# Optimization experiments

Measured on AMD Instinct MI355X. Metric: run time of the kernel, lower is better.

## Reference

```python
import jax, jax.numpy as jnp
import numpy as np

B, S, D = 8, 1024, 768
H, DH = 8, 96          # number_of_heads, head_outdim = D // H
DFF = 4 * D            # mlp hidden
EPS = 1e-5


def _p(key, shape, scale=0.02):
    return (jax.random.normal(key, shape, dtype=jnp.float32) * scale)


def setup_inputs() -> dict:
    key = jax.random.key(0)
    ks = jax.random.split(key, 16)
    return {
        "h": jax.random.normal(ks[0], (B, S, D), dtype=jnp.float32),
        "x": jax.random.normal(ks[1], (B, S, D), dtype=jnp.float32),
        # SLN 1: scalar gamma/beta + LayerNorm affine
        "g1": jnp.ones((), jnp.float32), "be1": jnp.zeros((), jnp.float32),
        "ln1_w": jnp.ones((D,), jnp.float32), "ln1_b": jnp.zeros((D,), jnp.float32),
        # SLN 2
        "g2": jnp.ones((), jnp.float32), "be2": jnp.zeros((), jnp.float32),
        "ln2_w": jnp.ones((D,), jnp.float32), "ln2_b": jnp.zeros((D,), jnp.float32),
        # MSA projections (stored as [in, out] for x @ W)
        "Wq": _p(ks[2], (D, H * DH)), "bq": jnp.zeros((H * DH,), jnp.float32),
        "Wk": _p(ks[3], (D, H * DH)), "bk": jnp.zeros((H * DH,), jnp.float32),
        "Wv": _p(ks[4], (D, H * DH)), "bv": jnp.zeros((H * DH,), jnp.float32),
        "Wo": _p(ks[5], (H * DH, D)), "bo": jnp.zeros((D,), jnp.float32),
        # MLP: D -> 4D -> D, relu
        "W1": _p(ks[6], (D, DFF)), "b1": jnp.zeros((DFF,), jnp.float32),
        "W2": _p(ks[7], (DFF, D)), "b2": jnp.zeros((D,), jnp.float32),
    }


def _sln(h, x, gamma, beta, w, b):
    # SLN(h, x) = gamma * x * LayerNorm(h) + beta * x
    mu = jnp.mean(h, axis=-1, keepdims=True)
    var = jnp.var(h, axis=-1, keepdims=True)
    ln = (h - mu) * jax.lax.rsqrt(var + EPS) * w + b
    return gamma * x * ln + beta * x


def _l2_msa(h, Wq, bq, Wk, bk, Wv, bv, Wo, bo):
    # L2-distance multi-head self-attention (lp=2)
    def heads(W, bias):
        y = h @ W + bias                      # [B,S,H*DH]
        return y.reshape(B, S, H, DH).transpose(0, 2, 1, 3)  # [B,H,S,DH]
    q, k, v = heads(Wq, bq), heads(Wk, bk), heads(Wv, bv)
    # pairwise L2 distances via the quadratic expansion (avoids [B,H,S,S,DH])
    q2 = jnp.sum(q * q, axis=-1)              # [B,H,S]
    k2 = jnp.sum(k * k, axis=-1)              # [B,H,S]
    qk = jnp.einsum("bhsd,bhtd->bhst", q, k)  # [B,H,S,S]
    d2 = jnp.maximum(q2[..., :, None] + k2[..., None, :] - 2.0 * qk, 0.0)
    dist = jnp.sqrt(d2)                       # cdist(q, k, p=2)
    attn = jax.nn.softmax(-dist / np.sqrt(DH), axis=-1)
    out = jnp.einsum("bhst,bhtd->bhsd", attn, v)  # [B,H,S,DH]
    out = out.transpose(0, 2, 1, 3).reshape(B, S, H * DH)
    return out @ Wo + bo


def reference(h, x, g1, be1, ln1_w, ln1_b, g2, be2, ln2_w, ln2_b,
              Wq, bq, Wk, bk, Wv, bv, Wo, bo, W1, b1, W2, b2):
    h1 = _sln(h, x, g1, be1, ln1_w, ln1_b)
    htmp = _l2_msa(h1, Wq, bq, Wk, bk, Wv, bv, Wo, bo) + h   # dropout_rate=0 -> identity
    h2 = _sln(htmp, x, g2, be2, ln2_w, ln2_b)
    hf = jax.nn.relu(h2 @ W1 + b1) @ W2 + b2 + htmp
    return (x, hf)
```

## Files before the change

kernel.cpp:

```cpp
#include <hip/hip_runtime.h>
#include <math.h>

#define B_ 8
#define S_ 1024
#define D_ 768
#define H_ 8
#define DH_ 96
#define DFF_ 3072
#define NTOK (B_*S_)
#define QKVW 2304
#define EPS_ 1e-5f

typedef __attribute__((ext_vector_type(4))) float f4;
typedef __attribute__((ext_vector_type(4))) int i4;
typedef __attribute__((ext_vector_type(8))) __bf16 bf16x8;
typedef __attribute__((ext_vector_type(4))) unsigned short us4;
typedef __attribute__((ext_vector_type(8))) unsigned short us8;

static __device__ __forceinline__ unsigned short f2bf(float f) {
    unsigned int u = __builtin_bit_cast(unsigned int, f);
    u += 0x7fffu + ((u >> 16) & 1u);
    return (unsigned short)(u >> 16);
}
static __device__ __forceinline__ float bf2f(unsigned short u) {
    unsigned int x = ((unsigned int)u) << 16;
    return __builtin_bit_cast(float, x);
}

#define GLOBAL_LOAD_LDS16(g, l) \
    __builtin_amdgcn_global_load_lds((const __attribute__((address_space(1))) unsigned int*)(g), \
                                     (__attribute__((address_space(3))) unsigned int*)(l), 16, 0, 0)

__global__ __launch_bounds__(192) void sln_kernel(
    const float* __restrict__ h, const float* __restrict__ x,
    const float* __restrict__ gamma, const float* __restrict__ beta,
    const float* __restrict__ w, const float* __restrict__ bvec,
    unsigned short* __restrict__ out_bf, float* __restrict__ xcopy)
{
    int row = blockIdx.x;
    int t = threadIdx.x;
    const float4* h4 = (const float4*)(h + (size_t)row * D_);
    const float4* x4 = (const float4*)(x + (size_t)row * D_);
    float4 hv = h4[t];
    float s  = hv.x + hv.y + hv.z + hv.w;
    float ss = hv.x*hv.x + hv.y*hv.y + hv.z*hv.z + hv.w*hv.w;
    #pragma unroll
    for (int off = 32; off > 0; off >>= 1) {
        s  += __shfl_down(s, off);
        ss += __shfl_down(ss, off);
    }
    __shared__ float red[2][3];
    int wid = t >> 6;
    if ((t & 63) == 0) { red[0][wid] = s; red[1][wid] = ss; }
    __syncthreads();
    float sum   = red[0][0] + red[0][1] + red[0][2];
    float sumsq = red[1][0] + red[1][1] + red[1][2];
    float mu  = sum * (1.0f / D_);
    float var = sumsq * (1.0f / D_) - mu * mu;
    float rstd = rsqrtf(var + EPS_);
    float g = gamma[0], be = beta[0];
    float4 wv = ((const float4*)w)[t];
    float4 bv = ((const float4*)bvec)[t];
    float4 xv = x4[t];
    us4 o;
    o.x = f2bf(xv.x * (g * ((hv.x - mu) * rstd * wv.x + bv.x) + be));
    o.y = f2bf(xv.y * (g * ((hv.y - mu) * rstd * wv.y + bv.y) + be));
    o.z = f2bf(xv.z * (g * ((hv.z - mu) * rstd * wv.z + bv.z) + be));
    o.w = f2bf(xv.w * (g * ((hv.w - mu) * rstd * wv.w + bv.w) + be));
    *(us4*)(out_bf + (size_t)row * D_ + t * 4) = o;
    if (xcopy) ((float4*)(xcopy + (size_t)row * D_))[t] = xv;
}

__global__ __launch_bounds__(256) void prep_all_kernel(
    const float* __restrict__ Wq, const float* __restrict__ Wk,
    const float* __restrict__ Wv, const float* __restrict__ Wo,
    const float* __restrict__ W1, const float* __restrict__ W2,
    const float* __restrict__ bq, const float* __restrict__ bk, const float* __restrict__ bv,
    unsigned short* __restrict__ Wqkvt, unsigned short* __restrict__ Wot,
    unsigned short* __restrict__ W1t, unsigned short* __restrict__ W2t,
    float* __restrict__ bqkv)
{
    int id = blockIdx.x;
    int tx = threadIdx.x, ty = threadIdx.y;
    if (id >= 6912) {
        int i = (id - 6912) * 256 + ty * 32 + tx;
        if (i < QKVW) {
            float v = (i < 768) ? bq[i] : (i < 1536) ? -2.f * bk[i - 768] : bv[i - 1536];
            bqkv[i] = v;
        }
        return;
    }
    const float* in; unsigned short* out; int K, N, nbx, rel;
    float scl = 1.f;
    if (id < 1728)      { int m = id / 576; rel = id % 576;
                          in = (m == 0) ? Wq : (m == 1) ? Wk : Wv;
                          if (m == 1) scl = -2.f;
                          out = Wqkvt + (size_t)m * 768 * 768; K = 768; N = 768; nbx = 24; }
    else if (id < 2304) { rel = id - 1728; in = Wo; out = Wot;  K = 768;  N = 768;  nbx = 24; }
    else if (id < 4608) { rel = id - 2304; in = W1; out = W1t;  K = 768;  N = 3072; nbx = 96; }
    else                { rel = id - 4608; in = W2; out = W2t;  K = 3072; N = 768;  nbx = 24; }
    int n0 = (rel % nbx) * 32, k0 = (rel / nbx) * 32;
    __shared__ float tile[32][33];
    #pragma unroll
    for (int r = 0; r < 4; r++)
        tile[ty + r * 8][tx] = in[(size_t)(k0 + ty + r * 8) * N + n0 + tx];
    __syncthreads();
    #pragma unroll
    for (int r = 0; r < 4; r++)
        out[(size_t)(n0 + ty + r * 8) * K + k0 + tx] = f2bf(scl * tile[tx][ty + r * 8]);
}

template<int OUT_BF16, int RELU>
__global__ __launch_bounds__(256) void gemm_mfma_kernel(
    const unsigned short* __restrict__ A, const unsigned short* __restrict__ Bt,
    const float* __restrict__ bias, const float* __restrict__ resid,
    void* __restrict__ Cout, int M, int N, int K)
{
    __shared__ unsigned short Asm[2][128 * 32];
    __shared__ unsigned short Bsm[2][128 * 32];

    int t = threadIdx.x;
    int lane = t & 63, wv = t >> 6;
    int wm = wv & 1, wn = wv >> 1;
    int l16 = lane & 15, quad = lane >> 4;

    int bm = blockIdx.x * 128;
    int bn = blockIdx.y * 128;

    const unsigned short* Abase = A  + (size_t)bm * K;
    const unsigned short* Bbase = Bt + (size_t)bn * K;

    int fl0 = t, fl1 = 256 + t;
    int r0 = fl0 >> 2, lg0 = (fl0 ^ (fl0 >> 3)) & 3;
    int r1 = fl1 >> 2, lg1 = (fl1 ^ (fl1 >> 3)) & 3;

    f4 acc[4][4] = {};

    GLOBAL_LOAD_LDS16(Abase + (size_t)r0 * K + lg0 * 8, &Asm[0][fl0 * 8]);
    GLOBAL_LOAD_LDS16(Abase + (size_t)r1 * K + lg1 * 8, &Asm[0][fl1 * 8]);
    GLOBAL_LOAD_LDS16(Bbase + (size_t)r0 * K + lg0 * 8, &Bsm[0][fl0 * 8]);
    GLOBAL_LOAD_LDS16(Bbase + (size_t)r1 * K + lg1 * 8, &Bsm[0][fl1 * 8]);
    __syncthreads();

    int nk = K >> 5;
    int cur = 0;
    for (int it = 0; it < nk; ++it) {
        if (it + 1 < nk) {
            int k0 = (it + 1) << 5;
            GLOBAL_LOAD_LDS16(Abase + (size_t)r0 * K + k0 + lg0 * 8, &Asm[cur ^ 1][fl0 * 8]);
            GLOBAL_LOAD_LDS16(Abase + (size_t)r1 * K + k0 + lg1 * 8, &Asm[cur ^ 1][fl1 * 8]);
            GLOBAL_LOAD_LDS16(Bbase + (size_t)r0 * K + k0 + lg0 * 8, &Bsm[cur ^ 1][fl0 * 8]);
            GLOBAL_LOAD_LDS16(Bbase + (size_t)r1 * K + k0 + lg1 * 8, &Bsm[cur ^ 1][fl1 * 8]);
        }

        bf16x8 xf[4], wf[4];
        #pragma unroll
        for (int i = 0; i < 4; i++) {
            int m = wm * 64 + i * 16 + l16;
            int p = (quad ^ (m >> 1)) & 3;
            xf[i] = __builtin_bit_cast(bf16x8, *(const i4*)&Asm[cur][m * 32 + p * 8]);
        }
        #pragma unroll
        for (int j = 0; j < 4; j++) {
            int n = wn * 64 + j * 16 + l16;
            int p = (quad ^ (n >> 1)) & 3;
            wf[j] = __builtin_bit_cast(bf16x8, *(const i4*)&Bsm[cur][n * 32 + p * 8]);
        }
        #pragma unroll
        for (int j = 0; j < 4; j++)
            #pragma unroll
            for (int i = 0; i < 4; i++)
                acc[j][i] = __builtin_amdgcn_mfma_f32_16x16x32_bf16(wf[j], xf[i], acc[j][i], 0, 0, 0);

        __syncthreads();
        cur ^= 1;
    }

    #pragma unroll
    for (int i = 0; i < 4; i++) {
        int rowg = bm + wm * 64 + i * 16 + l16;
        #pragma unroll
        for (int j = 0; j < 4; j++) {
            int colg0 = bn + wn * 64 + j * 16 + quad * 4;
            f4 v = acc[j][i];
            f4 b4 = *(const f4*)&bias[colg0];
            v += b4;
            if (RELU) {
                #pragma unroll
                for (int r = 0; r < 4; r++) v[r] = fmaxf(v[r], 0.f);
            }
            if (resid) {
                f4 r4 = *(const f4*)&resid[(size_t)rowg * N + colg0];
                v += r4;
            }
            if (OUT_BF16) {
                us4 o;
                o.x = f2bf(v[0]); o.y = f2bf(v[1]); o.z = f2bf(v[2]); o.w = f2bf(v[3]);
                *(us4*)((unsigned short*)Cout + (size_t)rowg * N + colg0) = o;
            } else {
                *(f4*)((float*)Cout + (size_t)rowg * N + colg0) = v;
            }
        }
    }
}

template<int OUT_BF16, int RELU>
__global__ __launch_bounds__(256) void gemm_mfma_n64_kernel(
    const unsigned short* __restrict__ A, const unsigned short* __restrict__ Bt,
    const float* __restrict__ bias, const float* __restrict__ resid,
    void* __restrict__ Cout, int M, int N, int K)
{
    __shared__ unsigned short Asm[2][128 * 64];
    __shared__ unsigned short Bsm[2][64 * 64];

    int t = threadIdx.x;
    int lane = t & 63, wv = t >> 6;
    int wm = wv & 1, wn = wv >> 1;
    int l16 = lane & 15, quad = lane >> 4;

    int bm = blockIdx.x * 128;
    int bn = blockIdx.y * 64;

    const unsigned short* Abase = A  + (size_t)bm * K;
    const unsigned short* Bbase = Bt + (size_t)bn * K;

    int ar[4], alg[4], br[2], blg[2];
    #pragma unroll
    for (int i = 0; i < 4; i++) {
        int fl = t + i * 256;
        ar[i] = fl >> 3; alg[i] = (fl ^ (fl >> 3)) & 7;
    }
    #pragma unroll
    for (int i = 0; i < 2; i++) {
        int fl = t + i * 256;
        br[i] = fl >> 3; blg[i] = (fl ^ (fl >> 3)) & 7;
    }

    f4 acc[2][4] = {};

    #pragma unroll
    for (int i = 0; i < 4; i++)
        GLOBAL_LOAD_LDS16(Abase + (size_t)ar[i] * K + alg[i] * 8, &Asm[0][(t + i * 256) * 8]);
    #pragma unroll
    for (int i = 0; i < 2; i++)
        GLOBAL_LOAD_LDS16(Bbase + (size_t)br[i] * K + blg[i] * 8, &Bsm[0][(t + i * 256) * 8]);
    __syncthreads();

    int nk = K >> 6;
    int cur = 0;
    for (int it = 0; it < nk; ++it) {
        if (it + 1 < nk) {
            int k0 = (it + 1) << 6;
            #pragma unroll
            for (int i = 0; i < 4; i++)
                GLOBAL_LOAD_LDS16(Abase + (size_t)ar[i] * K + k0 + alg[i] * 8, &Asm[cur ^ 1][(t + i * 256) * 8]);
            #pragma unroll
            for (int i = 0; i < 2; i++)
                GLOBAL_LOAD_LDS16(Bbase + (size_t)br[i] * K + k0 + blg[i] * 8, &Bsm[cur ^ 1][(t + i * 256) * 8]);
        }

        #pragma unroll
        for (int kk = 0; kk < 2; kk++) {
            bf16x8 xf[4], wf[2];
            #pragma unroll
            for (int i = 0; i < 4; i++) {
                int m = wm * 64 + i * 16 + l16;
                int p = ((kk * 4 + quad) ^ (m & 7)) & 7;
                xf[i] = __builtin_bit_cast(bf16x8, *(const i4*)&Asm[cur][m * 64 + p * 8]);
            }
            #pragma unroll
            for (int j = 0; j < 2; j++) {
                int n = wn * 32 + j * 16 + l16;
                int p = ((kk * 4 + quad) ^ (n & 7)) & 7;
                wf[j] = __builtin_bit_cast(bf16x8, *(const i4*)&Bsm[cur][n * 64 + p * 8]);
            }
            #pragma unroll
            for (int j = 0; j < 2; j++)
                #pragma unroll
                for (int i = 0; i < 4; i++)
                    acc[j][i] = __builtin_amdgcn_mfma_f32_16x16x32_bf16(wf[j], xf[i], acc[j][i], 0, 0, 0);
        }

        __syncthreads();
        cur ^= 1;
    }

    #pragma unroll
    for (int i = 0; i < 4; i++) {
        int rowg = bm + wm * 64 + i * 16 + l16;
        #pragma unroll
        for (int j = 0; j < 2; j++) {
            int colg0 = bn + wn * 32 + j * 16 + quad * 4;
            f4 v = acc[j][i];
            f4 b4 = *(const f4*)&bias[colg0];
            v += b4;
            if (RELU) {
                #pragma unroll
                for (int r = 0; r < 4; r++) v[r] = fmaxf(v[r], 0.f);
            }
            if (resid) {
                f4 r4 = *(const f4*)&resid[(size_t)rowg * N + colg0];
                v += r4;
            }
            if (OUT_BF16) {
                us4 o;
                o.x = f2bf(v[0]); o.y = f2bf(v[1]); o.z = f2bf(v[2]); o.w = f2bf(v[3]);
                *(us4*)((unsigned short*)Cout + (size_t)rowg * N + colg0) = o;
            } else {
                *(f4*)((float*)Cout + (size_t)rowg * N + colg0) = v;
            }
        }
    }
}

__global__ __launch_bounds__(256) void norms_kernel(
    const unsigned short* __restrict__ qkv, float* __restrict__ q2g, float* __restrict__ k2g)
{
    int row = blockIdx.x;
    int t = threadIdx.x;
    int hh = t >> 5, l32 = t & 31;
    const unsigned short* base = qkv + (size_t)row * QKVW + hh * DH_ + l32 * 3;
    float qs = 0.f, ks = 0.f;
    #pragma unroll
    for (int e = 0; e < 3; e++) {
        float qv = bf2f(base[e]);
        float kv = bf2f(base[768 + e]);
        qs += qv * qv; ks += kv * kv;
    }
    #pragma unroll
    for (int off = 16; off > 0; off >>= 1) {
        qs += __shfl_xor(qs, off, 32);
        ks += __shfl_xor(ks, off, 32);
    }
    if (l32 == 0) {
        int b = row >> 10, s = row & 1023;
        int idx = (b * H_ + hh) * S_ + s;
        q2g[idx] = qs; k2g[idx] = ks * 0.25f;
    }
}

__global__ __launch_bounds__(256) void vtrans_kernel(
    const unsigned short* __restrict__ qkv, unsigned short* __restrict__ vt)
{
    __shared__ unsigned short Vl[64][100];
    int blk = blockIdx.x;
    int bh = blk >> 4, kt = blk & 15;
    int b = bh >> 3, hh = bh & 7;
    int t = threadIdx.x;
    int key = t >> 2, qc = t & 3;
    const unsigned short* src = qkv + ((size_t)(b * S_ + kt * 64 + key)) * QKVW + 1536 + hh * DH_;
    #pragma unroll
    for (int i = 0; i < 3; i++) {
        int chunk = qc + i * 4;
        us8 v = *(const us8*)(src + chunk * 8);
        #pragma unroll
        for (int e = 0; e < 8; e++) Vl[key][chunk * 8 + e] = v[e];
    }
    __syncthreads();
    unsigned short* dst = vt + (size_t)blk * 7168;
    #pragma unroll
    for (int r = 0; r < 3; r++) {
        int c = r * 256 + t;
        int vd = c >> 3, kc = c & 7;
        us8 o;
        #pragma unroll
        for (int j = 0; j < 8; j++) o[j] = Vl[kc * 8 + j][vd];
        *(us8*)(dst + vd * 72 + kc * 8) = o;
    }
}

__global__ __launch_bounds__(256, 2) void attn_mfma_kernel(
    const unsigned short* __restrict__ qkv,
    const unsigned short* __restrict__ vt,
    const float* __restrict__ q2g, const float* __restrict__ k2g,
    unsigned short* __restrict__ outb)
{
    __shared__ unsigned short Klds[2][6144];
    __shared__ unsigned short Vlds[2][7168];
    __shared__ unsigned short Plds[4][2][16 * 72];

    int t = threadIdx.x;
    int lane = t & 63, w = t >> 6;
    int l16 = lane & 15, quad = lane >> 4;

    int bid = blockIdx.x;
    int slot = bid >> 3;
    int bh = (bid & 7) * 8 + (slot >> 3);
    int qt = slot & 7;
    int b = bh >> 3, hh = bh & 7;

    int qrowW = qt * 128 + w * 32;

    const unsigned short* qb = qkv + ((size_t)(b * S_ + qrowW)) * QKVW + hh * DH_;
    bf16x8 qf[2][3];
    #pragma unroll
    for (int f = 0; f < 2; f++)
        #pragma unroll
        for (int d = 0; d < 3; d++)
            qf[f][d] = __builtin_bit_cast(bf16x8,
                *(const i4*)(qb + (size_t)(f * 16 + l16) * QKVW + d * 32 + quad * 8));

    float q2n[2];
    #pragma unroll
    for (int f = 0; f < 2; f++)
        q2n[f] = q2g[bh * S_ + qrowW + f * 16 + l16];

    float lsum0 = 0.f, lsum1 = 0.f;
    f4 Oacc[2][6] = {};

    const float cexp = 0.14724445f;

    const unsigned short* kgb = qkv + ((size_t)(b * S_)) * QKVW + 768 + hh * DH_;
    const unsigned short* vgb0 = vt + (size_t)(bh * 16) * 7168;
    const float* k2base = k2g + bh * S_;

    int kkey = t & 63;
    #define ATTN_STAGE(bb, itv)                                                   \
        {                                                                         \
            _Pragma("unroll")                                                     \
            for (int r = 0; r < 3; r++) {                                         \
                int c = r * 256 + t;                                              \
                int dc = c >> 6;                                                  \
                GLOBAL_LOAD_LDS16(kgb + ((size_t)((itv) * 64 + kkey)) * QKVW + dc * 8, \
                                  &Klds[bb][c * 8]);                              \
            }                                                                     \
            const unsigned short* vgb = vgb0 + (size_t)(itv) * 7168;              \
            _Pragma("unroll")                                                     \
            for (int r = 0; r < 3; r++)                                           \
                GLOBAL_LOAD_LDS16(vgb + (r * 256 + t) * 8, &Vlds[bb][(r * 256 + t) * 8]); \
            if (t < 128)                                                          \
                GLOBAL_LOAD_LDS16(vgb + (768 + t) * 8, &Vlds[bb][(768 + t) * 8]); \
        }

    ATTN_STAGE(0, 0);
    __syncthreads();

    for (int it = 0; it < 16; it++) {
        int cur = it & 1;
        if (it) __syncthreads();
        if (it + 1 < 16) ATTN_STAGE(cur ^ 1, it + 1);

        float4 k2f[4];
        #pragma unroll
        for (int kt2 = 0; kt2 < 4; kt2++)
            k2f[kt2] = *(const float4*)(k2base + it * 64 + kt2 * 16 + quad * 4);

        const unsigned short* kB = &Klds[cur][quad * 512 + l16 * 8];
        #pragma unroll
        for (int kt2 = 0; kt2 < 4; kt2++) {
            const unsigned short* kp = kB + kt2 * 128;
            bf16x8 kf0 = __builtin_bit_cast(bf16x8, *(const i4*)(kp));
            bf16x8 kf1 = __builtin_bit_cast(bf16x8, *(const i4*)(kp + 2048));
            bf16x8 kf2 = __builtin_bit_cast(bf16x8, *(const i4*)(kp + 4096));
            #pragma unroll
            for (int f = 0; f < 2; f++) {
                f4 a = {k2f[kt2].x + q2n[f], k2f[kt2].y + q2n[f],
                        k2f[kt2].z + q2n[f], k2f[kt2].w + q2n[f]};
                a = __builtin_amdgcn_mfma_f32_16x16x32_bf16(kf0, qf[f][0], a, 0, 0, 0);
                a = __builtin_amdgcn_mfma_f32_16x16x32_bf16(kf1, qf[f][1], a, 0, 0, 0);
                a = __builtin_amdgcn_mfma_f32_16x16x32_bf16(kf2, qf[f][2], a, 0, 0, 0);
                #pragma unroll
                for (int r2 = 0; r2 < 4; r2++) {
                    float d2 = fmaxf(a[r2], 0.f);
                    float p = exp2f(-__builtin_amdgcn_sqrtf(d2) * cexp);
                    if (f == 0) lsum0 += p; else lsum1 += p;
                    a[r2] = p;
                }
                unsigned int plo, phi;
                asm("v_cvt_pk_bf16_f32 %0, %1, %2" : "=v"(plo) : "v"(a[0]), "v"(a[1]));
                asm("v_cvt_pk_bf16_f32 %0, %1, %2" : "=v"(phi) : "v"(a[2]), "v"(a[3]));
                uint2 pkd; pkd.x = plo; pkd.y = phi;
                *(uint2*)&Plds[w][f][l16 * 72 + kt2 * 16 + quad * 4] = pkd;
            }
        }
        bf16x8 pa[2][2];
        #pragma unroll
        for (int f = 0; f < 2; f++) {
            pa[f][0] = __builtin_bit_cast(bf16x8, *(const i4*)&Plds[w][f][l16 * 72 + quad * 8]);
            pa[f][1] = __builtin_bit_cast(bf16x8, *(const i4*)&Plds[w][f][l16 * 72 + 32 + quad * 8]);
        }
        #pragma unroll
        for (int vtl = 0; vtl < 6; vtl++) {
            bf16x8 vf0 = __builtin_bit_cast(bf16x8, *(const i4*)&Vlds[cur][(vtl * 16 + l16) * 72 + quad * 8]);
            bf16x8 vf1 = __builtin_bit_cast(bf16x8, *(const i4*)&Vlds[cur][(vtl * 16 + l16) * 72 + 32 + quad * 8]);
            #pragma unroll
            for (int f = 0; f < 2; f++) {
                Oacc[f][vtl] = __builtin_amdgcn_mfma_f32_16x16x32_bf16(pa[f][0], vf0, Oacc[f][vtl], 0, 0, 0);
                Oacc[f][vtl] = __builtin_amdgcn_mfma_f32_16x16x32_bf16(pa[f][1], vf1, Oacc[f][vtl], 0, 0, 0);
            }
        }
    }
    #pragma unroll
    for (int f = 0; f < 2; f++) {
        float ls = (f == 0) ? lsum0 : lsum1;
        ls += __shfl_xor(ls, 16, 64);
        ls += __shfl_xor(ls, 32, 64);
        float inv_l = 1.f / ls;
        f4 iv;
        #pragma unroll
        for (int r2 = 0; r2 < 4; r2++)
            iv[r2] = __shfl(inv_l, quad * 4 + r2, 64);
        #pragma unroll
        for (int vtl = 0; vtl < 6; vtl++)
            #pragma unroll
            for (int r2 = 0; r2 < 4; r2++) {
                int row = b * S_ + qrowW + f * 16 + quad * 4 + r2;
                outb[(size_t)row * D_ + hh * DH_ + vtl * 16 + l16] = f2bf(Oacc[f][vtl][r2] * iv[r2]);
            }
    }
    #undef ATTN_STAGE
}

extern "C" void kernel_launch(void* const* d_in, const int* in_sizes, int n_in,
                              void* d_out, int out_size, void* d_ws, size_t ws_size,
                              hipStream_t stream)
{
    const float* h    = (const float*)d_in[0];
    const float* x    = (const float*)d_in[1];
    const float* g1   = (const float*)d_in[2];
    const float* be1  = (const float*)d_in[3];
    const float* ln1w = (const float*)d_in[4];
    const float* ln1b = (const float*)d_in[5];
    const float* g2   = (const float*)d_in[6];
    const float* be2  = (const float*)d_in[7];
    const float* ln2w = (const float*)d_in[8];
    const float* ln2b = (const float*)d_in[9];
    const float* Wq   = (const float*)d_in[10];
    const float* bq   = (const float*)d_in[11];
    const float* Wk   = (const float*)d_in[12];
    const float* bk   = (const float*)d_in[13];
    const float* Wv   = (const float*)d_in[14];
    const float* bv   = (const float*)d_in[15];
    const float* Wo   = (const float*)d_in[16];
    const float* bo   = (const float*)d_in[17];
    const float* W1   = (const float*)d_in[18];
    const float* b1   = (const float*)d_in[19];
    const float* W2   = (const float*)d_in[20];
    const float* b2   = (const float*)d_in[21];

    float* out = (float*)d_out;
    char* wsb = (char*)d_ws;
    const size_t ND = (size_t)NTOK * D_;

    size_t off = 0;
    unsigned short* W1t = (unsigned short*)(wsb + off); off += 4718592;
    unsigned short* W2t = (unsigned short*)(wsb + off); off += 4718592;
    float* bqkv = (float*)(wsb + off);                  off += 16384;
    float* htmp = (float*)(wsb + off);                  off += ND * 4;
    float* q2g  = (float*)(wsb + off);                  off += (size_t)B_ * H_ * S_ * 4;
    float* k2g  = (float*)(wsb + off);                  off += (size_t)B_ * H_ * S_ * 4;
    unsigned short* h2b = (unsigned short*)(wsb + off); off += ND * 2;
    size_t pool0 = off;
    unsigned short* Wqkvt = (unsigned short*)(wsb + off); off += 3538944;
    unsigned short* Wot   = (unsigned short*)(wsb + off); off += 1179648;
    unsigned short* h1b   = (unsigned short*)(wsb + off); off += ND * 2;
    unsigned short* vtg   = (unsigned short*)(wsb + off); off += (size_t)1024 * 14336;
    unsigned short* qkvb  = (unsigned short*)(wsb + off); off += (size_t)NTOK * QKVW * 2;
    unsigned short* attnb   = h1b;
    unsigned short* hiddenb = (unsigned short*)(wsb + pool0);

    prep_all_kernel<<<6921, dim3(32, 8), 0, stream>>>(
        Wq, Wk, Wv, Wo, W1, W2, bq, bk, bv, Wqkvt, Wot, W1t, W2t, bqkv);

    sln_kernel<<<NTOK, 192, 0, stream>>>(h, x, g1, be1, ln1w, ln1b, h1b, out);

    gemm_mfma_kernel<1, 0><<<dim3(NTOK/128, QKVW/128), 256, 0, stream>>>(
        h1b, Wqkvt, bqkv, nullptr, qkvb, NTOK, QKVW, D_);

    norms_kernel<<<NTOK, 256, 0, stream>>>(qkvb, q2g, k2g);
    vtrans_kernel<<<1024, 256, 0, stream>>>(qkvb, vtg);

    attn_mfma_kernel<<<512, 256, 0, stream>>>(qkvb, vtg, q2g, k2g, attnb);

    gemm_mfma_n64_kernel<0, 0><<<dim3(NTOK/128, D_/64), 256, 0, stream>>>(
        attnb, Wot, bo, h, htmp, NTOK, D_, D_);

    sln_kernel<<<NTOK, 192, 0, stream>>>(htmp, x, g2, be2, ln2w, ln2b, h2b, nullptr);

    gemm_mfma_kernel<1, 1><<<dim3(NTOK/128, DFF_/128), 256, 0, stream>>>(
        h2b, W1t, b1, nullptr, hiddenb, NTOK, DFF_, D_);
    gemm_mfma_n64_kernel<0, 0><<<dim3(NTOK/128, D_/64), 256, 0, stream>>>(
        hiddenb, W2t, b2, htmp, out + ND, NTOK, D_, DFF_);

    (void)in_sizes; (void)n_in; (void)out_size; (void)ws_size;
}
```

Before: 425.1 us.

## Fold softmax scale into Q/K weights, fuse norms into V transpose, stage k2 in LDS

The softmax distance scale is now folded into the Q and K weights and biases at prep time, so q2/k2 come out pre-scaled and the attention inner loop drops one multiply per score. The separate norms kernel is merged into the V-transpose kernel, which saves one launch and one pass over Q/K. The attention kernel stages k2 into LDS with async loads instead of global float4 reads every iteration, and adds s_setprio around the MFMA blocks. Folding the scale into bf16 weights changes rounding slightly, and fabs replaces the clamp on negative d2.

```diff
diff --git a/kernel.cpp b/kernel.cpp
--- a/kernel.cpp
+++ b/kernel.cpp
@@ -10,6 +10,7 @@
 #define NTOK (B_*S_)
 #define QKVW 2304
 #define EPS_ 1e-5f
+#define CEXP_ 0.14724445f
 
 typedef __attribute__((ext_vector_type(4))) float f4;
 typedef __attribute__((ext_vector_type(4))) int i4;
@@ -85,7 +86,8 @@
     if (id >= 6912) {
         int i = (id - 6912) * 256 + ty * 32 + tx;
         if (i < QKVW) {
-            float v = (i < 768) ? bq[i] : (i < 1536) ? -2.f * bk[i - 768] : bv[i - 1536];
+            float v = (i < 768) ? CEXP_ * bq[i]
+                    : (i < 1536) ? -2.f * CEXP_ * bk[i - 768] : bv[i - 1536];
             bqkv[i] = v;
         }
         return;
@@ -94,7 +96,8 @@
     float scl = 1.f;
     if (id < 1728)      { int m = id / 576; rel = id % 576;
                           in = (m == 0) ? Wq : (m == 1) ? Wk : Wv;
-                          if (m == 1) scl = -2.f;
+                          if (m == 0) scl = CEXP_;
+                          if (m == 1) scl = -2.f * CEXP_;
                           out = Wqkvt + (size_t)m * 768 * 768; K = 768; N = 768; nbx = 24; }
     else if (id < 2304) { rel = id - 1728; in = Wo; out = Wot;  K = 768;  N = 768;  nbx = 24; }
     else if (id < 4608) { rel = id - 2304; in = W1; out = W1t;  K = 768;  N = 3072; nbx = 96; }
@@ -313,34 +316,9 @@
     }
 }
 
-__global__ __launch_bounds__(256) void norms_kernel(
-    const unsigned short* __restrict__ qkv, float* __restrict__ q2g, float* __restrict__ k2g)
-{
-    int row = blockIdx.x;
-    int t = threadIdx.x;
-    int hh = t >> 5, l32 = t & 31;
-    const unsigned short* base = qkv + (size_t)row * QKVW + hh * DH_ + l32 * 3;
-    float qs = 0.f, ks = 0.f;
-    #pragma unroll
-    for (int e = 0; e < 3; e++) {
-        float qv = bf2f(base[e]);
-        float kv = bf2f(base[768 + e]);
-        qs += qv * qv; ks += kv * kv;
-    }
-    #pragma unroll
-    for (int off = 16; off > 0; off >>= 1) {
-        qs += __shfl_xor(qs, off, 32);
-        ks += __shfl_xor(ks, off, 32);
-    }
-    if (l32 == 0) {
-        int b = row >> 10, s = row & 1023;
-        int idx = (b * H_ + hh) * S_ + s;
-        q2g[idx] = qs; k2g[idx] = ks * 0.25f;
-    }
-}
-
-__global__ __launch_bounds__(256) void vtrans_kernel(
-    const unsigned short* __restrict__ qkv, unsigned short* __restrict__ vt)
+__global__ __launch_bounds__(256) void vtrans_norms_kernel(
+    const unsigned short* __restrict__ qkv, unsigned short* __restrict__ vt,
+    float* __restrict__ q2g, float* __restrict__ k2g)
 {
     __shared__ unsigned short Vl[64][100];
     int blk = blockIdx.x;
@@ -348,7 +326,25 @@
     int b = bh >> 3, hh = bh & 7;
     int t = threadIdx.x;
     int key = t >> 2, qc = t & 3;
-    const unsigned short* src = qkv + ((size_t)(b * S_ + kt * 64 + key)) * QKVW + 1536 + hh * DH_;
+    const unsigned short* tok = qkv + ((size_t)(b * S_ + kt * 64 + key)) * QKVW + hh * DH_;
+    float qs = 0.f, ks = 0.f;
+    #pragma unroll
+    for (int i = 0; i < 3; i++) {
+        us8 qv = *(const us8*)(tok + (qc * 3 + i) * 8);
+        us8 kv = *(const us8*)(tok + 768 + (qc * 3 + i) * 8);
+        #pragma unroll
+        for (int e = 0; e < 8; e++) {
+            float qf = bf2f(qv[e]), kf = bf2f(kv[e]);
+            qs += qf * qf; ks += kf * kf;
+        }
+    }
+    qs += __shfl_xor(qs, 1, 4); qs += __shfl_xor(qs, 2, 4);
+    ks += __shfl_xor(ks, 1, 4); ks += __shfl_xor(ks, 2, 4);
+    if (qc == 0) {
+        int idx = (b * H_ + hh) * S_ + kt * 64 + key;
+        q2g[idx] = qs; k2g[idx] = ks * 0.25f;
+    }
+    const unsigned short* src = tok + 1536;
     #pragma unroll
     for (int i = 0; i < 3; i++) {
         int chunk = qc + i * 4;
@@ -377,6 +373,7 @@
 {
     __shared__ unsigned short Klds[2][6144];
     __shared__ unsigned short Vlds[2][7168];
+    __shared__ float k2lds[2][64];
     __shared__ unsigned short Plds[4][2][16 * 72];
 
     int t = threadIdx.x;
@@ -407,8 +404,6 @@
 
     float lsum0 = 0.f, lsum1 = 0.f;
     f4 Oacc[2][6] = {};
-
-    const float cexp = 0.14724445f;
 
     const unsigned short* kgb = qkv + ((size_t)(b * S_)) * QKVW + 768 + hh * DH_;
     const unsigned short* vgb0 = vt + (size_t)(bh * 16) * 7168;
@@ -430,6 +425,8 @@
                 GLOBAL_LOAD_LDS16(vgb + (r * 256 + t) * 8, &Vlds[bb][(r * 256 + t) * 8]); \
             if (t < 128)                                                          \
                 GLOBAL_LOAD_LDS16(vgb + (768 + t) * 8, &Vlds[bb][(768 + t) * 8]); \
+            if (t < 16)                                                           \
+                GLOBAL_LOAD_LDS16(k2base + (itv) * 64 + t * 4, &k2lds[bb][t * 4]); \
         }
 
     ATTN_STAGE(0, 0);
@@ -439,11 +436,6 @@
         int cur = it & 1;
         if (it) __syncthreads();
         if (it + 1 < 16) ATTN_STAGE(cur ^ 1, it + 1);
-
-        float4 k2f[4];
-        #pragma unroll
-        for (int kt2 = 0; kt2 < 4; kt2++)
-            k2f[kt2] = *(const float4*)(k2base + it * 64 + kt2 * 16 + quad * 4);
 
         const unsigned short* kB = &Klds[cur][quad * 512 + l16 * 8];
         #pragma unroll
@@ -452,17 +444,18 @@
             bf16x8 kf0 = __builtin_bit_cast(bf16x8, *(const i4*)(kp));
             bf16x8 kf1 = __builtin_bit_cast(bf16x8, *(const i4*)(kp + 2048));
             bf16x8 kf2 = __builtin_bit_cast(bf16x8, *(const i4*)(kp + 4096));
+            f4 kk = *(const f4*)&k2lds[cur][kt2 * 16 + quad * 4];
             #pragma unroll
             for (int f = 0; f < 2; f++) {
-                f4 a = {k2f[kt2].x + q2n[f], k2f[kt2].y + q2n[f],
-                        k2f[kt2].z + q2n[f], k2f[kt2].w + q2n[f]};
+                f4 a = {kk[0] + q2n[f], kk[1] + q2n[f], kk[2] + q2n[f], kk[3] + q2n[f]};
+                __builtin_amdgcn_s_setprio(1);
                 a = __builtin_amdgcn_mfma_f32_16x16x32_bf16(kf0, qf[f][0], a, 0, 0, 0);
                 a = __builtin_amdgcn_mfma_f32_16x16x32_bf16(kf1, qf[f][1], a, 0, 0, 0);
                 a = __builtin_amdgcn_mfma_f32_16x16x32_bf16(kf2, qf[f][2], a, 0, 0, 0);
+                __builtin_amdgcn_s_setprio(0);
                 #pragma unroll
                 for (int r2 = 0; r2 < 4; r2++) {
-                    float d2 = fmaxf(a[r2], 0.f);
-                    float p = exp2f(-__builtin_amdgcn_sqrtf(d2) * cexp);
+                    float p = exp2f(-__builtin_amdgcn_sqrtf(__builtin_fabsf(a[r2])));
                     if (f == 0) lsum0 += p; else lsum1 += p;
                     a[r2] = p;
                 }
@@ -479,6 +472,7 @@
             pa[f][0] = __builtin_bit_cast(bf16x8, *(const i4*)&Plds[w][f][l16 * 72 + quad * 8]);
             pa[f][1] = __builtin_bit_cast(bf16x8, *(const i4*)&Plds[w][f][l16 * 72 + 32 + quad * 8]);
         }
+        __builtin_amdgcn_s_setprio(1);
         #pragma unroll
         for (int vtl = 0; vtl < 6; vtl++) {
             bf16x8 vf0 = __builtin_bit_cast(bf16x8, *(const i4*)&Vlds[cur][(vtl * 16 + l16) * 72 + quad * 8]);
@@ -489,6 +483,7 @@
                 Oacc[f][vtl] = __builtin_amdgcn_mfma_f32_16x16x32_bf16(pa[f][1], vf1, Oacc[f][vtl], 0, 0, 0);
             }
         }
+        __builtin_amdgcn_s_setprio(0);
     }
     #pragma unroll
     for (int f = 0; f < 2; f++) {
@@ -567,8 +562,7 @@
     gemm_mfma_kernel<1, 0><<<dim3(NTOK/128, QKVW/128), 256, 0, stream>>>(
         h1b, Wqkvt, bqkv, nullptr, qkvb, NTOK, QKVW, D_);
 
-    norms_kernel<<<NTOK, 256, 0, stream>>>(qkvb, q2g, k2g);
-    vtrans_kernel<<<1024, 256, 0, stream>>>(qkvb, vtg);
+    vtrans_norms_kernel<<<1024, 256, 0, stream>>>(qkvb, vtg, q2g, k2g);
 
     attn_mfma_kernel<<<512, 256, 0, stream>>>(qkvb, vtg, q2g, k2g, attnb);
 
```

Result: faster. 404.7 us (-4.8%).
